# Kernel tuning notes

Measured on AMD Instinct MI355X. Metric: run time of the kernel, lower is better.

The kernel has to match this reference:

```python
import jax, jax.numpy as jnp
import numpy as np
from jax.ops import segment_sum, segment_max

B = 512          # parcels (batch of graphs)
P = 200          # poi nodes per parcel
N = B * P        # total poi nodes
E_POI = N * 16   # intra-parcel poi graph edges
HID = 256
IN_CH = 64
HEADS = 3
OUT = 12
T0 = 0.9
SLOPE = 0.2      # GATConv leaky_relu negative slope
NODE_GRAPH = jnp.arange(N, dtype=jnp.int32) // P  # poi node -> parcel id
ARANGE_N = jnp.arange(N, dtype=jnp.int32)


def setup_inputs() -> dict:
    key = jax.random.key(0)
    ks = jax.random.split(key, 24)
    g = lambda i, shape: jax.random.normal(ks[i], shape, jnp.float32) * 0.05
    # poi graph edges constrained within each parcel block
    src0 = jax.random.randint(ks[0], (E_POI,), 0, N, dtype=jnp.int32)
    off = jax.random.randint(ks[1], (E_POI,), 0, P, dtype=jnp.int32)
    return dict(
        g_poi_features=jax.random.normal(ks[2], (N, IN_CH), jnp.float32),
        img_feat=jax.random.normal(ks[3], (B, 2048), jnp.float32),
        edge_src=src0,
        edge_dst=(src0 // P) * P + off,
        W_gcn1=g(4, (IN_CH, HID)), b_gcn1=jnp.zeros((HID,), jnp.float32),
        W_gcn2=g(5, (HID, HID)), b_gcn2=jnp.zeros((HID,), jnp.float32),
        W_hrs=g(6, (2048, HID)), b_hrs=jnp.zeros((HID,), jnp.float32),
        W_proj_hrs=g(7, (HID, HID)), b_proj_hrs=jnp.zeros((HID,), jnp.float32),
        W_proj_poi=g(8, (HID, HID)), b_proj_poi=jnp.zeros((HID,), jnp.float32),
        W_gat_in=g(9, (HID, HEADS * HID)), al_in=g(10, (HEADS, HID)), ar_in=g(11, (HEADS, HID)),
        W_gat_with=g(12, (HID, HEADS * HID)), al_with=g(13, (HEADS, HID)), ar_with=g(14, (HEADS, HID)),
        W_hrsgnn=g(15, (HID, HID)),
        W_poignn=g(16, (HID, HID)),
        W_fc=g(17, (4 * HID, OUT)), b_fc=jnp.zeros((OUT,), jnp.float32),
    )


def _gcn(x, src, dst, W, b):
    # DGL GraphConv, norm='both', self-loops added
    s = jnp.concatenate([src, ARANGE_N])
    d = jnp.concatenate([dst, ARANGE_N])
    deg = segment_sum(jnp.ones_like(s, jnp.float32), d, num_segments=N)
    norm = jax.lax.rsqrt(jnp.maximum(deg, 1.0))
    h = (x @ W) * norm[:, None]
    m = segment_sum(h[s], d, num_segments=N)
    return m * norm[:, None] + b


def _gat(h_src, h_dst, src, dst, n_dst, W, al, ar):
    # DGL GATConv math: shared fc, additive attention, edge-softmax over dst
    fs = (h_src @ W).reshape(-1, HEADS, HID)
    fd = (h_dst @ W).reshape(-1, HEADS, HID)
    el = (fs * al).sum(-1)   # [n_src, H]
    er = (fd * ar).sum(-1)   # [n_dst, H]
    e = el[src] + er[dst]
    e = jnp.where(e > 0, e, SLOPE * e)
    m = segment_max(e, dst, num_segments=n_dst)
    w = jnp.exp(e - m[dst])
    z = segment_sum(w, dst, num_segments=n_dst)
    alpha = w / (z[dst] + 1e-9)
    out = segment_sum(fs[src] * alpha[:, :, None], dst, num_segments=n_dst)
    return out.mean(1)  # mean over heads (parcel_output.mean(1) in source)


def _mean_nodes(x):
    # dgl.mean_nodes over uniform-size batched graphs
    return segment_sum(x, NODE_GRAPH, num_segments=B) / P


def reference(g_poi_features, img_feat, edge_src, edge_dst,
              W_gcn1, b_gcn1, W_gcn2, b_gcn2, W_hrs, b_hrs,
              W_proj_hrs, b_proj_hrs, W_proj_poi, b_proj_poi,
              W_gat_in, al_in, ar_in, W_gat_with, al_with, ar_with,
              W_hrsgnn, W_poignn, W_fc, b_fc):
    # hrs_encoder: ResNet50 backbone modeled as precomputed 2048-d feats + replaced fc
    hrs = img_feat @ W_hrs + b_hrs                                  # [B, HID]
    # poi_encoder: 2-layer GCN over batched poi graph
    x = jax.nn.relu(_gcn(g_poi_features, edge_src, edge_dst, W_gcn1, b_gcn1))
    poi_nodes = _gcn(x, edge_src, edge_dst, W_gcn2, b_gcn2)         # [N, HID]
    poi_pooled = _mean_nodes(poi_nodes)                             # [B, HID]
    # mid-level fused similarity
    med = jnp.concatenate([hrs, poi_pooled], axis=1)
    med = med / jnp.linalg.norm(med, axis=1, keepdims=True)
    med_output = (med @ med.T + 1.0) / 2.0                          # [B, B]
    # UniSimGraph: GCN on thresholded parcel-similarity graph
    adj = jnp.where(med_output >= T0, 1.0, 0.0)
    adj = jnp.maximum(adj, jnp.eye(B, dtype=jnp.float32))
    dinv = jax.lax.rsqrt(adj.sum(1))
    nadj = adj * dinv[:, None] * dinv[None, :]
    hrs_agg = jax.nn.relu(nadj @ (hrs @ W_hrsgnn))                  # [B, HID]
    poi_agg = jax.nn.relu(nadj @ (poi_pooled @ W_poignn))           # [B, HID]
    # getHetGraph: bipartite poi<->parcel GAT, 3 heads, sum-aggregate, head-mean
    ph = hrs @ W_proj_hrs + b_proj_hrs                              # parcel feats
    pp = poi_nodes @ W_proj_poi + b_proj_poi                        # poi feats
    poi2img = _gat(pp, ph, ARANGE_N, NODE_GRAPH, B, W_gat_in, al_in, ar_in)      # [B, HID]
    img2poi = _gat(ph, pp, NODE_GRAPH, ARANGE_N, N, W_gat_with, al_with, ar_with)  # [N, HID]
    img2poi_pooled = _mean_nodes(img2poi)                           # [B, HID]
    # MutualAgg concat order: [img2poi, poi2poi(=poi_agg), poi2img, img2img(=hrs_agg)]
    agg = jnp.concatenate([img2poi_pooled, poi_agg, poi2img, hrs_agg], axis=1)
    output = agg @ W_fc + b_fc                                      # [B, OUT]
    return (output, med_output)
```

## Files before the change

kernel.cpp:

```cpp
#include <hip/hip_runtime.h>
#include <hip/hip_bf16.h>
#include <math.h>


#define N_NODES 102400
#define B_PAR   512
#define P_NODES 200
#define E_EDGES 1638400
#define HIDF    256

typedef __attribute__((ext_vector_type(8))) short bf16x8;
typedef __attribute__((ext_vector_type(4))) float f32x4;

__device__ __forceinline__ unsigned short f2bf(float x) {
    unsigned u = __builtin_bit_cast(unsigned, x);
    u += 0x7fffu + ((u >> 16) & 1u);
    return (unsigned short)(u >> 16);
}
__device__ __forceinline__ float bf2f(unsigned short h) {
    return __builtin_bit_cast(float, (unsigned)h << 16);
}
__device__ __forceinline__ int lds_off(int row, int kbyte) {
    return row * 128 + ((((kbyte >> 4) ^ (row & 7)) << 4) | (kbyte & 15));
}
template<bool BF16SRC>
__device__ __forceinline__ bf16x8 load_row8(const void* p, size_t elemoff) {
    if constexpr (BF16SRC) {
        return *(const bf16x8*)((const unsigned short*)p + elemoff);
    } else {
        const float* ap = (const float*)p + elemoff;
        float4 lo = *(const float4*)ap;
        float4 hi = *(const float4*)(ap + 4);
        union { bf16x8 v; unsigned short u[8]; } pk;
        pk.u[0] = f2bf(lo.x); pk.u[1] = f2bf(lo.y);
        pk.u[2] = f2bf(lo.z); pk.u[3] = f2bf(lo.w);
        pk.u[4] = f2bf(hi.x); pk.u[5] = f2bf(hi.y);
        pk.u[6] = f2bf(hi.z); pk.u[7] = f2bf(hi.w);
        return pk.v;
    }
}
__device__ __forceinline__ bf16x8 u8x8_to_bf16(uint2 w) {
    union { bf16x8 v; unsigned short u[8]; } r;
#pragma unroll
    for (int b = 0; b < 4; ++b) {
        r.u[b]     = (unsigned short)(__builtin_bit_cast(unsigned,
                        (float)((w.x >> (8 * b)) & 255u)) >> 16);
        r.u[4 + b] = (unsigned short)(__builtin_bit_cast(unsigned,
                        (float)((w.y >> (8 * b)) & 255u)) >> 16);
    }
    return r.v;
}

template<bool ABF16, bool BBF16, int OMODE, int SCMODE, bool BIASF, bool RELUF>
__global__ __launch_bounds__(512, 2) void mm256_k(
    const void* __restrict__ Ain, const void* __restrict__ Bin,
    void* __restrict__ Cout, int M, int Nc, int K,
    const float* __restrict__ scale, const float* __restrict__ bias)
{
    __shared__ bf16x8 smem_v[4096];
    unsigned char* Asm = (unsigned char*)smem_v;
    unsigned char* Bsm = Asm + 32768;

    const int tid  = threadIdx.x;
    const int m0   = blockIdx.y * 256;
    const int n0   = blockIdx.x * 256;
    const int sr   = tid >> 3, sc = tid & 7;
    const int lane = tid & 63;
    const int wave = tid >> 6;
    const int wm   = wave >> 2, wn = wave & 3;
    const int frow = lane & 15;
    const int fko  = (lane >> 4) << 4;

    f32x4 acc[8][4];
    const f32x4 fz = {0.f, 0.f, 0.f, 0.f};
#pragma unroll
    for (int i = 0; i < 8; ++i)
#pragma unroll
        for (int j = 0; j < 4; ++j) acc[i][j] = fz;

    bf16x8 areg[4], breg[4];
    auto load_tiles = [&](int k0) {
#pragma unroll
        for (int i = 0; i < 4; ++i) {
            int row = sr + 64 * i;
            areg[i] = load_row8<ABF16>(Ain, (size_t)(m0 + row) * K + k0 + sc * 8);
            breg[i] = load_row8<BBF16>(Bin, (size_t)(n0 + row) * K + k0 + sc * 8);
        }
    };

    load_tiles(0);
    for (int k0 = 0; k0 < K; k0 += 64) {
        __syncthreads();
#pragma unroll
        for (int i = 0; i < 4; ++i) {
            *(bf16x8*)(Asm + lds_off(sr + 64 * i, sc * 16)) = areg[i];
            *(bf16x8*)(Bsm + lds_off(sr + 64 * i, sc * 16)) = breg[i];
        }
        __syncthreads();
        if (k0 + 64 < K) load_tiles(k0 + 64);
#pragma unroll
        for (int ks = 0; ks < 2; ++ks) {
            const int kb = ks * 64 + fko;
            bf16x8 bfr[4];
#pragma unroll
            for (int t = 0; t < 4; ++t)
                bfr[t] = *(const bf16x8*)(Bsm + lds_off(wn * 64 + t * 16 + frow, kb));
#pragma unroll
            for (int mi = 0; mi < 8; ++mi) {
                bf16x8 af = *(const bf16x8*)(Asm + lds_off(wm * 128 + mi * 16 + frow, kb));
#pragma unroll
                for (int ni = 0; ni < 4; ++ni)
                    acc[mi][ni] = __builtin_amdgcn_mfma_f32_16x16x32_bf16(
                        af, bfr[ni], acc[mi][ni], 0, 0, 0);
            }
        }
    }

    const int r4 = (lane >> 4) << 2;
#pragma unroll
    for (int mi = 0; mi < 8; ++mi) {
#pragma unroll
        for (int ni = 0; ni < 4; ++ni) {
            int col = n0 + wn * 64 + ni * 16 + frow;
#pragma unroll
            for (int j = 0; j < 4; ++j) {
                int row = m0 + wm * 128 + mi * 16 + r4 + j;
                float v = acc[mi][ni][j];
                if (SCMODE == 1) v *= scale[row];
                if (SCMODE == 2) v *= scale[col];
                if (BIASF)       v += bias[col];
                if (RELUF)       v = fmaxf(v, 0.f);
                if (OMODE == 0) {
                    ((float*)Cout)[(size_t)row * Nc + col] = v;
                } else if (OMODE == 1) {
                    ((unsigned short*)Cout)[(size_t)row * Nc + col] = f2bf(v);
                } else {
                    int p = col / 200, r = col - p * 200;
                    ((unsigned short*)Cout)[((size_t)p * 256 + row) * 256 + r] = f2bf(v);
                }
            }
        }
    }
}

__global__ __launch_bounds__(512, 2) void agg256_k(
    const unsigned char* __restrict__ Adj, const unsigned short* __restrict__ Yt,
    unsigned short* __restrict__ Outb, const float* __restrict__ nrm,
    const float* __restrict__ bias, int relu)
{
    __shared__ bf16x8 smem_v[4096];
    unsigned char* Asm = (unsigned char*)smem_v;
    unsigned char* Bsm = Asm + 32768;

    const int tid  = threadIdx.x;
    const int p    = blockIdx.x;
    const int sr   = tid >> 3, sc = tid & 7;
    const int lane = tid & 63;
    const int wave = tid >> 6;
    const int wm   = wave >> 2, wn = wave & 3;
    const int frow = lane & 15;
    const int fko  = (lane >> 4) << 4;
    const size_t abase = (size_t)p * 65536;
    const size_t ybase = (size_t)p * 65536;

    f32x4 acc[8][4];
    const f32x4 fz = {0.f, 0.f, 0.f, 0.f};
#pragma unroll
    for (int i = 0; i < 8; ++i)
#pragma unroll
        for (int j = 0; j < 4; ++j) acc[i][j] = fz;

    uint2  awreg[4];
    bf16x8 breg[4];
    auto load_tiles = [&](int k0) {
#pragma unroll
        for (int i = 0; i < 4; ++i) {
            int row = sr + 64 * i;
            awreg[i] = *(const uint2*)(Adj + abase + (size_t)row * 256 + k0 + sc * 8);
            breg[i]  = *(const bf16x8*)(Yt + ybase + (size_t)row * 256 + k0 + sc * 8);
        }
    };

    load_tiles(0);
#pragma unroll
    for (int t4 = 0; t4 < 4; ++t4) {
        __syncthreads();
#pragma unroll
        for (int i = 0; i < 4; ++i) {
            *(bf16x8*)(Asm + lds_off(sr + 64 * i, sc * 16)) = u8x8_to_bf16(awreg[i]);
            *(bf16x8*)(Bsm + lds_off(sr + 64 * i, sc * 16)) = breg[i];
        }
        __syncthreads();
        if (t4 < 3) load_tiles((t4 + 1) * 64);
#pragma unroll
        for (int ks = 0; ks < 2; ++ks) {
            const int kb = ks * 64 + fko;
            bf16x8 bfr[4];
#pragma unroll
            for (int t = 0; t < 4; ++t)
                bfr[t] = *(const bf16x8*)(Bsm + lds_off(wn * 64 + t * 16 + frow, kb));
#pragma unroll
            for (int mi = 0; mi < 8; ++mi) {
                bf16x8 af = *(const bf16x8*)(Asm + lds_off(wm * 128 + mi * 16 + frow, kb));
#pragma unroll
                for (int ni = 0; ni < 4; ++ni)
                    acc[mi][ni] = __builtin_amdgcn_mfma_f32_16x16x32_bf16(
                        af, bfr[ni], acc[mi][ni], 0, 0, 0);
            }
        }
    }

    const int r4 = (lane >> 4) << 2;
#pragma unroll
    for (int mi = 0; mi < 8; ++mi) {
#pragma unroll
        for (int ni = 0; ni < 4; ++ni) {
            int col = wn * 64 + ni * 16 + frow;
#pragma unroll
            for (int j = 0; j < 4; ++j) {
                int d = wm * 128 + mi * 16 + r4 + j;
                if (d < 200) {
                    int g = p * 200 + d;
                    float v = acc[mi][ni][j] * nrm[g] + bias[col];
                    if (relu) v = fmaxf(v, 0.f);
                    Outb[(size_t)g * 256 + col] = f2bf(v);
                }
            }
        }
    }
}

__global__ __launch_bounds__(512) void agg1_k(
    const unsigned char* __restrict__ Adj, const unsigned short* __restrict__ Xnt,
    unsigned short* __restrict__ AX)
{
    __shared__ bf16x8 smem_v[2560];
    unsigned char* Asm = (unsigned char*)smem_v;
    unsigned char* Bsm = Asm + 32768;

    const int tid  = threadIdx.x;
    const int p    = blockIdx.x;
    const int arow = tid >> 1, ah = tid & 1;
    const int brow = tid >> 3, sc = tid & 7;
    const int lane = tid & 63;
    const int wave = tid >> 6;
    const int frow = lane & 15;
    const int fko  = (lane >> 4) << 4;
    const size_t abase = (size_t)p * 65536;
    const size_t xbase = (size_t)p * 16384;

    f32x4 acc[2][4];
    const f32x4 fz = {0.f, 0.f, 0.f, 0.f};
#pragma unroll
    for (int i = 0; i < 2; ++i)
#pragma unroll
        for (int j = 0; j < 4; ++j) acc[i][j] = fz;

    uint4  aw[2];
    bf16x8 bg;
    auto load_tiles = [&](int k0) {
        const uint4* ap = (const uint4*)(Adj + abase + (size_t)arow * 256 + k0 + ah * 32);
        aw[0] = ap[0];
        aw[1] = ap[1];
        bg = *(const bf16x8*)(Xnt + xbase + (size_t)brow * 256 + k0 + sc * 8);
    };

    load_tiles(0);
#pragma unroll
    for (int t4 = 0; t4 < 4; ++t4) {
        __syncthreads();
        {
            uint2 l0 = {aw[0].x, aw[0].y}, h0 = {aw[0].z, aw[0].w};
            uint2 l1 = {aw[1].x, aw[1].y}, h1 = {aw[1].z, aw[1].w};
            int base = ah * 64;
            *(bf16x8*)(Asm + lds_off(arow, base +  0)) = u8x8_to_bf16(l0);
            *(bf16x8*)(Asm + lds_off(arow, base + 16)) = u8x8_to_bf16(h0);
            *(bf16x8*)(Asm + lds_off(arow, base + 32)) = u8x8_to_bf16(l1);
            *(bf16x8*)(Asm + lds_off(arow, base + 48)) = u8x8_to_bf16(h1);
            *(bf16x8*)(Bsm + lds_off(brow, sc * 16)) = bg;
        }
        __syncthreads();
        if (t4 < 3) load_tiles((t4 + 1) * 64);
#pragma unroll
        for (int ks = 0; ks < 2; ++ks) {
            const int kb = ks * 64 + fko;
            bf16x8 bfr[4];
#pragma unroll
            for (int t = 0; t < 4; ++t)
                bfr[t] = *(const bf16x8*)(Bsm + lds_off(t * 16 + frow, kb));
#pragma unroll
            for (int mi = 0; mi < 2; ++mi) {
                bf16x8 af = *(const bf16x8*)(Asm + lds_off(wave * 32 + mi * 16 + frow, kb));
#pragma unroll
                for (int ni = 0; ni < 4; ++ni)
                    acc[mi][ni] = __builtin_amdgcn_mfma_f32_16x16x32_bf16(
                        af, bfr[ni], acc[mi][ni], 0, 0, 0);
            }
        }
    }

    const int r4 = (lane >> 4) << 2;
#pragma unroll
    for (int mi = 0; mi < 2; ++mi) {
#pragma unroll
        for (int ni = 0; ni < 4; ++ni) {
            int col = ni * 16 + frow;
#pragma unroll
            for (int j = 0; j < 4; ++j) {
                int d = wave * 32 + mi * 16 + r4 + j;
                if (d < 200)
                    AX[((size_t)(p * 200 + d)) * 64 + col] = f2bf(acc[mi][ni][j]);
            }
        }
    }
}

__global__ __launch_bounds__(256) void xt_k(const float* __restrict__ gp,
                                            const float* __restrict__ nrm,
                                            unsigned short* __restrict__ Xnt)
{
    __shared__ unsigned short lsh[64][264];
    const int p = blockIdx.x, tid = threadIdx.x;
    for (int idx = tid; idx < 256 * 16; idx += 256) {
        int s = idx >> 4, kc = idx & 15;
        float4 v = {0.f, 0.f, 0.f, 0.f};
        float nr = 0.f;
        if (s < 200) {
            v = *(const float4*)(gp + ((size_t)(p * 200 + s)) * 64 + kc * 4);
            nr = nrm[p * 200 + s];
        }
        lsh[kc * 4 + 0][s] = f2bf(v.x * nr);
        lsh[kc * 4 + 1][s] = f2bf(v.y * nr);
        lsh[kc * 4 + 2][s] = f2bf(v.z * nr);
        lsh[kc * 4 + 3][s] = f2bf(v.w * nr);
    }
    __syncthreads();
    for (int idx = tid; idx < 64 * 32; idx += 256) {
        int k = idx >> 5, ch = idx & 31;
        uint4 o = *(const uint4*)(&lsh[k][ch * 8]);
        *(uint4*)(Xnt + (size_t)p * 16384 + k * 256 + ch * 8) = o;
    }
}

template<bool ABF16, bool BBF16, int OMODE, bool BIASF, bool RELUF,
         bool MEDOUT, int KCHUNK>
__global__ __launch_bounds__(256) void mm64_k(
    const void* __restrict__ Ain, const void* __restrict__ Bin,
    void* __restrict__ Cout, int M, int Nc, int K,
    const float* __restrict__ bias, float alpha)
{
    __shared__ bf16x8 smem_v[1024];
    unsigned char* Asm = (unsigned char*)smem_v;
    unsigned char* Bsm = Asm + 8192;

    const int tid  = threadIdx.x;
    const int m0   = blockIdx.y * 64;
    const int n0   = blockIdx.x * 64;
    const int sr   = tid >> 3, sc = tid & 7;
    const int lane = tid & 63;
    const int wm   = (tid >> 7) & 1, wn = (tid >> 6) & 1;
    const int frow = lane & 15;
    const int fko  = (lane >> 4) << 4;

    int kbeg = 0, kend = K;
    float* Cf = (float*)Cout;
    if (KCHUNK > 0) {
        kbeg = blockIdx.z * KCHUNK; kend = kbeg + KCHUNK;
        Cf += (size_t)blockIdx.z * M * Nc;
    }

    f32x4 acc[2][2];
    const f32x4 fz = {0.f, 0.f, 0.f, 0.f};
#pragma unroll
    for (int i = 0; i < 2; ++i)
#pragma unroll
        for (int j = 0; j < 2; ++j) acc[i][j] = fz;

    bf16x8 areg[2], breg[2];
    auto load_tiles = [&](int k0) {
#pragma unroll
        for (int i = 0; i < 2; ++i) {
            int row = sr + 32 * i;
            areg[i] = load_row8<ABF16>(Ain, (size_t)(m0 + row) * K + k0 + sc * 8);
            breg[i] = load_row8<BBF16>(Bin, (size_t)(n0 + row) * K + k0 + sc * 8);
        }
    };

    load_tiles(kbeg);
    for (int k0 = kbeg; k0 < kend; k0 += 64) {
        __syncthreads();
#pragma unroll
        for (int i = 0; i < 2; ++i) {
            *(bf16x8*)(Asm + lds_off(sr + 32 * i, sc * 16)) = areg[i];
            *(bf16x8*)(Bsm + lds_off(sr + 32 * i, sc * 16)) = breg[i];
        }
        __syncthreads();
        if (k0 + 64 < kend) load_tiles(k0 + 64);
#pragma unroll
        for (int ks = 0; ks < 2; ++ks) {
            const int kb = ks * 64 + fko;
            bf16x8 af[2], bfr[2];
#pragma unroll
            for (int t = 0; t < 2; ++t)
                af[t] = *(const bf16x8*)(Asm + lds_off(wm * 32 + t * 16 + frow, kb));
#pragma unroll
            for (int t = 0; t < 2; ++t)
                bfr[t] = *(const bf16x8*)(Bsm + lds_off(wn * 32 + t * 16 + frow, kb));
#pragma unroll
            for (int mi = 0; mi < 2; ++mi)
#pragma unroll
                for (int ni = 0; ni < 2; ++ni)
                    acc[mi][ni] = __builtin_amdgcn_mfma_f32_16x16x32_bf16(
                        af[mi], bfr[ni], acc[mi][ni], 0, 0, 0);
        }
    }

    const int r4 = (lane >> 4) << 2;
#pragma unroll
    for (int mi = 0; mi < 2; ++mi) {
#pragma unroll
        for (int ni = 0; ni < 2; ++ni) {
            int col = n0 + wn * 32 + ni * 16 + frow;
#pragma unroll
// ... 54 lines not shown
__global__ __launch_bounds__(256) void prep_k(
    const float* __restrict__ W1, const float* __restrict__ W2,
    const float* __restrict__ Whg,
    const float* __restrict__ Wpg, const float* __restrict__ Whrs,
    const float* __restrict__ Wgin, const float* __restrict__ Wgw,
    const float* __restrict__ Wph, const float* __restrict__ img,
    unsigned short* __restrict__ W1t, unsigned short* __restrict__ W2t,
    unsigned short* __restrict__ Whgt,
    unsigned short* __restrict__ Wpgt, unsigned short* __restrict__ Whrst,
    unsigned short* __restrict__ Wgint, unsigned short* __restrict__ Wmt,
    unsigned short* __restrict__ Wphb, unsigned short* __restrict__ imgb)
{
    int b = blockIdx.x, tid = threadIdx.x;
    if (b < 64) {
        int id = b * 256 + tid; int n = id >> 6, k = id & 63;
        W1t[id] = f2bf(W1[(size_t)k * 256 + n]);
    } else if (b < 320) {
        int id = (b - 64) * 256 + tid; int n = id >> 8, k = id & 255;
        W2t[id] = f2bf(W2[(size_t)k * 256 + n]);
    } else if (b < 576) {
        int id = (b - 320) * 256 + tid; int n = id >> 8, k = id & 255;
        Whgt[id] = f2bf(Whg[(size_t)k * 256 + n]);
    } else if (b < 832) {
        int id = (b - 576) * 256 + tid; int n = id >> 8, k = id & 255;
        Wpgt[id] = f2bf(Wpg[(size_t)k * 256 + n]);
    } else if (b < 2880) {
        int id = (b - 832) * 256 + tid; int n = id >> 11, k = id & 2047;
        Whrst[id] = f2bf(Whrs[(size_t)k * 256 + n]);
    } else if (b < 3648) {
        int id = (b - 2880) * 256 + tid; int j = id / 768, k2 = id - j * 768;
        int t = k2 & 255, h = k2 >> 8;
        Wgint[id] = f2bf(Wgin[(size_t)t * 768 + h * 256 + j]);
    } else if (b < 3904) {
        int id = (b - 3648) * 256 + tid; int j = id >> 8, t = id & 255;
        const float c3 = (1.f / 3.f) * (1.f / (1.f + 1e-9f));
        float s = Wgw[(size_t)t * 768 + j] + Wgw[(size_t)t * 768 + 256 + j] +
                  Wgw[(size_t)t * 768 + 512 + j];
        Wmt[id] = f2bf(s * c3);
    } else if (b < 4160) {
        int id = (b - 3904) * 256 + tid;
        Wphb[id] = f2bf(Wph[id]);
    } else {
        int id = (b - 4160) * 256 + tid;
        imgb[id] = f2bf(img[id]);
    }
}

__global__ __launch_bounds__(256) void wpg_k(
    const float* __restrict__ Wpp, const float* __restrict__ Wgin,
    const float* __restrict__ bpp,
    unsigned short* __restrict__ WpG, float* __restrict__ bgg)
{
    __shared__ float wsh[256];
    const int b = blockIdx.x, j = threadIdx.x;
    if (b < 768) {
        int h = b >> 8, c = b & 255;
        wsh[j] = Wpp[(size_t)c * 256 + j];
        __syncthreads();
        float acc = 0.f;
        for (int t = 0; t < 256; ++t)
            acc += wsh[t] * Wgin[(size_t)t * 768 + h * 256 + j];
        WpG[(size_t)j * 768 + h * 256 + c] = f2bf(acc);
    } else {
        float s = 0.f;
        for (int h = 0; h < 3; ++h)
            for (int t = 0; t < 256; ++t)
                s += bpp[t] * Wgin[(size_t)t * 768 + h * 256 + j];
        bgg[j] = s * (1.f / 3.f);
    }
}

__global__ __launch_bounds__(256) void hrs_reduce_k(
    const float* __restrict__ part, const float* __restrict__ bhrs,
    float* __restrict__ hrs, unsigned short* __restrict__ hrsb)
{
    int id = blockIdx.x * 256 + threadIdx.x;
    float s = bhrs[id & 255];
#pragma unroll
    for (int z = 0; z < 8; ++z) s += part[(size_t)z * 131072 + id];
    hrs[id] = s;
    hrsb[id] = f2bf(s);
}

__global__ __launch_bounds__(256) void pool_k(const unsigned short* __restrict__ X,
                                              float* __restrict__ Pl,
                                              unsigned short* __restrict__ Plb)
{
    __shared__ float sh[2048];
    const int b = blockIdx.x, tid = threadIdx.x;
    const int cg = tid & 31, rg = tid >> 5;
    const size_t base = (size_t)b * P_NODES * HIDF + cg * 8;
    float acc[8] = {};
    for (int n = rg; n < P_NODES; n += 8) {
        union { uint4 q; unsigned short u[8]; } v;
        v.q = *(const uint4*)(X + base + (size_t)n * HIDF);
#pragma unroll
        for (int j = 0; j < 8; ++j) acc[j] += bf2f(v.u[j]);
    }
#pragma unroll
    for (int j = 0; j < 8; ++j) sh[rg * 256 + cg * 8 + j] = acc[j];
    __syncthreads();
    float s = 0.f;
#pragma unroll
    for (int r = 0; r < 8; ++r) s += sh[r * 256 + tid];
    s *= (1.f / 200.f);
    Pl[(size_t)b * 256 + tid] = s;
    Plb[(size_t)b * 256 + tid] = f2bf(s);
}

__global__ __launch_bounds__(256) void med_build_k(
    const float* __restrict__ hrs, const float* __restrict__ pool,
    unsigned short* __restrict__ medb)
{
    __shared__ float red[256];
    int b = blockIdx.x, f = threadIdx.x;
    float v0 = hrs[(size_t)b * 256 + f];
    float v1 = pool[(size_t)b * 256 + f];
    red[f] = v0 * v0 + v1 * v1;
    __syncthreads();
    for (int s = 128; s > 0; s >>= 1) {
        if (f < s) red[f] += red[f + s];
        __syncthreads();
    }
    float inv = rsqrtf(red[0]);
    medb[(size_t)b * 512 + f]       = f2bf(v0 * inv);
    medb[(size_t)b * 512 + 256 + f] = f2bf(v1 * inv);
}

__global__ __launch_bounds__(256) void dinv_k(const float* __restrict__ mo,
                                              float* __restrict__ dinv)
{
    __shared__ int red[256];
    int i = blockIdx.x, t = threadIdx.x;
    int c = 0;
    for (int j = t; j < 512; j += 256) c += (mo[(size_t)i * 512 + j] >= 0.9f) ? 1 : 0;
    red[t] = c; __syncthreads();
    for (int s = 128; s > 0; s >>= 1) {
        if (t < s) red[t] += red[t + s];
        __syncthreads();
    }
    if (t == 0) dinv[i] = rsqrtf((float)red[0]);
}

__global__ __launch_bounds__(256) void nadj_k(const float* __restrict__ mo,
                                              const float* __restrict__ dinv,
                                              unsigned short* __restrict__ nadjb)
{
    int i = blockIdx.x, t = threadIdx.x;
    float di = dinv[i];
    for (int j = t; j < 512; j += 256) {
        float a = (mo[(size_t)i * 512 + j] >= 0.9f || j == i) ? 1.f : 0.f;
        nadjb[(size_t)i * 512 + j] = f2bf(a * di * dinv[j]);
    }
}

__global__ __launch_bounds__(256) void uv1_k(
    const float* __restrict__ Wgin, const float* __restrict__ al,
    const float* __restrict__ ar,
    float* __restrict__ u2, float* __restrict__ v2)
{
    const int wave = threadIdx.x >> 6, lane = threadIdx.x & 63;
    const int task = blockIdx.x * 4 + wave;
    const int k = task / 3, h = task - k * 3;
    float4 w = *(const float4*)(Wgin + (size_t)k * 768 + h * 256 + lane * 4);
    float4 a = *(const float4*)(al + h * 256 + lane * 4);
    float4 r = *(const float4*)(ar + h * 256 + lane * 4);
    float su = w.x * a.x + w.y * a.y + w.z * a.z + w.w * a.w;
    float sv = w.x * r.x + w.y * r.y + w.z * r.z + w.w * r.w;
#pragma unroll
    for (int o = 32; o > 0; o >>= 1) {
        su += __shfl_xor(su, o);
        sv += __shfl_xor(sv, o);
    }
    if (lane == 0) { u2[task] = su; v2[task] = sv; }
}

__global__ __launch_bounds__(256) void uv2_k(
    const float* __restrict__ Wph, const float* __restrict__ Wpp,
    const float* __restrict__ bph, const float* __restrict__ bpp,
    const unsigned short* __restrict__ Wmt,
    const float* __restrict__ u2, const float* __restrict__ v2,
    float* __restrict__ vv2, float* __restrict__ wu,
    float* __restrict__ bc, float* __restrict__ erb, float* __restrict__ eb0)
{
    __shared__ float ush[768], vsh[768];
    const int tid = threadIdx.x;
    for (int i = tid; i < 768; i += 256) { ush[i] = u2[i]; vsh[i] = v2[i]; }
    __syncthreads();
    const int wave = tid >> 6, lane = tid & 63;
    const int task = blockIdx.x * 4 + wave;
    float s = 0.f;
    if (task < 1536) {
// ... 88 lines not shown
        float sm = 0.f;
        for (int n = lane; n < P_NODES; n += 64) sm += expf(esh[n * 3 + wave] - mx);
        for (int o = 32; o > 0; o >>= 1) sm += __shfl_xor(sm, o);
        if (lane == 0) { mz[wave] = mx; mz[4 + wave] = sm; }
    }
    __syncthreads();

    for (int it = tid; it < 600; it += 256) {
        int h = it % 3;
        ash[it] = expf(esh[it] - mz[h]) / (mz[4 + h] + 1e-9f);
    }
    __syncthreads();

    float a0 = 0.f, a1 = 0.f, a2 = 0.f;
    for (int n = 0; n < P_NODES; ++n) {
        float vv = bf2f(PN[(base + n) * HIDF + tid]);
        a0 += ash[n * 3 + 0] * vv;
        a1 += ash[n * 3 + 1] * vv;
        a2 += ash[n * 3 + 2] * vv;
    }
    q[((size_t)p * 3 + 0) * 256 + tid] = a0;
    q[((size_t)p * 3 + 1) * 256 + tid] = a1;
    q[((size_t)p * 3 + 2) * 256 + tid] = a2;
}

__global__ __launch_bounds__(256) void final_k(
    const float* __restrict__ i2p, const float* __restrict__ hpagg,
    const float* __restrict__ p2i,
    const float* __restrict__ Wfc, const float* __restrict__ bfc,
    float* __restrict__ out)
{
    int id = blockIdx.x * 256 + threadIdx.x;
    if (id >= B_PAR * 12) return;
    int b = id / 12, o = id % 12;
    float acc = bfc[o];
    const float* s0 = i2p + (size_t)b * 256;
    const float* s1 = hpagg + (size_t)b * 512 + 256;
    const float* s2 = p2i + (size_t)b * 256;
    const float* s3 = hpagg + (size_t)b * 512;
    for (int k = 0; k < 256; ++k) {
        acc += s0[k] * Wfc[(size_t)(0 * 256 + k) * 12 + o];
        acc += s1[k] * Wfc[(size_t)(1 * 256 + k) * 12 + o];
        acc += s2[k] * Wfc[(size_t)(2 * 256 + k) * 12 + o];
        acc += s3[k] * Wfc[(size_t)(3 * 256 + k) * 12 + o];
    }
    out[id] = acc;
}

extern "C" void kernel_launch(void* const* d_in, const int* in_sizes, int n_in,
                              void* d_out, int out_size, void* d_ws, size_t ws_size,
                              hipStream_t stream)
{
    const float* g_poi = (const float*)d_in[0];
    const float* img   = (const float*)d_in[1];
    const int*   esrc  = (const int*)d_in[2];
    const int*   edst  = (const int*)d_in[3];
    const float* W1    = (const float*)d_in[4];
    const float* b1    = (const float*)d_in[5];
    const float* W2    = (const float*)d_in[6];
    const float* b2    = (const float*)d_in[7];
    const float* Whrs  = (const float*)d_in[8];
    const float* bhrs  = (const float*)d_in[9];
    const float* Wph   = (const float*)d_in[10];
    const float* bph   = (const float*)d_in[11];
    const float* Wpp   = (const float*)d_in[12];
    const float* bpp   = (const float*)d_in[13];
    const float* Wgin  = (const float*)d_in[14];
    const float* alin  = (const float*)d_in[15];
    const float* arin  = (const float*)d_in[16];
    const float* Wgw   = (const float*)d_in[17];
    const float* Whg   = (const float*)d_in[20];
    const float* Wpg   = (const float*)d_in[21];
    const float* Wfc   = (const float*)d_in[22];
    const float* bfc   = (const float*)d_in[23];

    float* out     = (float*)d_out;
    float* med_out = out + B_PAR * 12;

    char* ws = (char*)d_ws;
    size_t off = 0;
    auto take = [&](size_t bytes) { void* pv = ws + off; off += (bytes + 255) & ~(size_t)255; return pv; };

    unsigned char*  adj8 = (unsigned char*)take((size_t)B_PAR * 256 * 256);
    unsigned short* Yt   = (unsigned short*)take((size_t)B_PAR * 256 * 256 * 2);
    unsigned short* Xnt  = Yt;
    unsigned short* XPN  = (unsigned short*)take((size_t)N_NODES * 256 * 2);
    unsigned short* AX   = (unsigned short*)take((size_t)N_NODES * 64 * 2);
    float*          part = (float*)take((size_t)8 * 512 * 256 * 4);

    unsigned short* W1t   = (unsigned short*)take(256 * 64 * 2);
    unsigned short* W2t   = (unsigned short*)take(256 * 256 * 2);
    unsigned short* Whgt  = (unsigned short*)take(256 * 256 * 2);
    unsigned short* Wpgt  = (unsigned short*)take(256 * 256 * 2);
    unsigned short* Whrst = (unsigned short*)take((size_t)256 * 2048 * 2);
    unsigned short* Wgint = (unsigned short*)take((size_t)256 * 768 * 2);
    unsigned short* Wmt   = (unsigned short*)take(256 * 256 * 2);
    unsigned short* Wphb  = (unsigned short*)take(256 * 256 * 2);
    unsigned short* WcT   = (unsigned short*)take(256 * 256 * 2);
    unsigned short* WpG   = (unsigned short*)take((size_t)256 * 768 * 2);
    unsigned short* imgb  = (unsigned short*)take((size_t)512 * 2048 * 2);
    unsigned short* hrsb  = (unsigned short*)take((size_t)B_PAR * 256 * 2);
    unsigned short* poolb = (unsigned short*)take((size_t)B_PAR * 256 * 2);
    unsigned short* medb  = (unsigned short*)take((size_t)B_PAR * 512 * 2);
    unsigned short* nadjb = (unsigned short*)take((size_t)B_PAR * 512 * 2);
    unsigned short* Tcatt = (unsigned short*)take((size_t)512 * 512 * 2);
    float* nrm   = (float*)take((size_t)N_NODES * 4);
    float* hrs   = (float*)take((size_t)B_PAR * 256 * 4);
    float* pool  = (float*)take((size_t)B_PAR * 256 * 4);
    float* dinv  = (float*)take((size_t)B_PAR * 4);
    float* hpagg = (float*)take((size_t)B_PAR * 512 * 4);
    float* u2    = (float*)take(768 * 4);
    float* v2    = (float*)take(768 * 4);
    float* wu    = (float*)take(768 * 4);
    float* vv2   = (float*)take(768 * 4);
    float* erb   = (float*)take(16);
    float* eb0   = (float*)take(16);
    float* bc    = (float*)take(256 * 4);
    float* bgg   = (float*)take(256 * 4);
    float* er    = (float*)take((size_t)B_PAR * 3 * 4);
    float* q     = (float*)take((size_t)B_PAR * 768 * 4);
    float* p2i   = (float*)take((size_t)B_PAR * 256 * 4);
    float* i2p   = (float*)take((size_t)B_PAR * 256 * 4);
    (void)ws_size; (void)in_sizes; (void)n_in; (void)out_size;

    hipMemsetAsync(adj8, 0, (size_t)B_PAR * 256 * 256, stream);
    prep_k<<<8256, 256, 0, stream>>>(W1, W2, Whg, Wpg, Whrs, Wgin, Wgw,
        Wph, img, W1t, W2t, Whgt, Wpgt, Whrst, Wgint, Wmt, Wphb, imgb);
    edge_diag_k<<<(E_EDGES + N_NODES) / 256, 256, 0, stream>>>(esrc, edst, adj8);
    norm2_k<<<N_NODES / 256, 256, 0, stream>>>(adj8, nrm);
    wpg_k<<<769, 256, 0, stream>>>(Wpp, Wgin, bpp, WpG, bgg);

    mm64_k<true, true, 0, false, false, false, 256>
        <<<dim3(4, 8, 8), 256, 0, stream>>>(imgb, Whrst, part, 512, 256, 2048,
            nullptr, 1.f);
    hrs_reduce_k<<<512, 256, 0, stream>>>(part, bhrs, hrs, hrsb);

    uv1_k<<<192, 256, 0, stream>>>(Wgin, alin, arin, u2, v2);
    uv2_k<<<450, 256, 0, stream>>>(Wph, Wpp, bph, bpp, Wmt, u2, v2,
                                   vv2, wu, bc, erb, eb0);
    er2_k<<<384, 256, 0, stream>>>(hrs, vv2, erb, eb0, er);
    mm64_k<true, true, 1, false, false, false, 0>
        <<<dim3(4, 4), 256, 0, stream>>>(Wmt, Wphb, WcT, 256, 256, 256,
            nullptr, 1.f);

    xt_k<<<512, 256, 0, stream>>>(g_poi, nrm, Xnt);
    agg1_k<<<512, 512, 0, stream>>>(adj8, Xnt, AX);
    mm256_k<true, true, 1, 1, true, true>
        <<<dim3(1, 400), 512, 0, stream>>>(AX, W1t, XPN, N_NODES, 256, 64,
            nrm, b1);

    mm256_k<true, true, 2, 2, false, false>
        <<<dim3(400, 1), 512, 0, stream>>>(W2t, XPN, Yt, 256, N_NODES, 256,
            nrm, nullptr);
    agg256_k<<<512, 512, 0, stream>>>(adj8, Yt, XPN, nrm, b2, 0);

    pool_k<<<B_PAR, 256, 0, stream>>>(XPN, pool, poolb);

    med_build_k<<<B_PAR, 256, 0, stream>>>(hrs, pool, medb);
    mm64_k<true, true, 0, false, false, true, 0>
        <<<dim3(8, 8), 256, 0, stream>>>(medb, medb, med_out, 512, 512, 512,
            nullptr, 0.5f);

    dinv_k<<<B_PAR, 256, 0, stream>>>(med_out, dinv);
    nadj_k<<<B_PAR, 256, 0, stream>>>(med_out, dinv, nadjb);
    mm64_k<true, true, 1, false, false, false, 0>
        <<<dim3(8, 4), 256, 0, stream>>>(Whgt, hrsb, Tcatt, 256, 512, 256,
            nullptr, 1.f);
    mm64_k<true, true, 1, false, false, false, 0>
        <<<dim3(8, 4), 256, 0, stream>>>(Wpgt, poolb, Tcatt + (size_t)256 * 512,
            256, 512, 256, nullptr, 1.f);
    mm64_k<true, true, 0, false, true, false, 0>
        <<<dim3(8, 8), 256, 0, stream>>>(nadjb, Tcatt, hpagg, 512, 512, 512,
            nullptr, 1.f);

    gat_poi2img_k<<<B_PAR, 256, 0, stream>>>(XPN, wu, er, q);
    mm64_k<false, true, 0, true, false, false, 0>
        <<<dim3(4, 8), 256, 0, stream>>>(q, WpG, p2i, 512, 256, 768,
            bgg, 1.f / 3.f);

    mm64_k<true, true, 0, true, false, false, 0>
        <<<dim3(4, 8), 256, 0, stream>>>(hrsb, WcT, i2p, 512, 256, 256,
            bc, 1.f);

    final_k<<<24, 256, 0, stream>>>(i2p, hpagg, p2i, Wfc, bfc, out);
}
```

Measured before the change: 428.2 us.

## Fuse GCN layers into per-parcel kernels with in-LDS aggregation and pooling

Replaces the xt/agg1/mm256/agg256/pool kernel chain with two per-parcel kernels. gcnA does transpose-normalize, adjacency aggregation and the W1 projection with bias/relu in one block and writes a normalized transposed layer-1 output. gcnB aggregates over the adjacency first and then multiplies by W2 in K-chunks, with mean pooling fused into its epilogue. This removes intermediate global buffers and several launches, and cuts the K extent to 224 instead of 256. In exchange each block carries heavy register and LDS use and fine-grained syncs, which may lower occupancy.

Result: faster. 391.6 us (-8.5%).

```diff
diff --git a/kernel.cpp b/kernel.cpp
--- a/kernel.cpp
+++ b/kernel.cpp
@@ -51,277 +51,42 @@
     return r.v;
 }
 
-template<bool ABF16, bool BBF16, int OMODE, int SCMODE, bool BIASF, bool RELUF>
-__global__ __launch_bounds__(512, 2) void mm256_k(
-    const void* __restrict__ Ain, const void* __restrict__ Bin,
-    void* __restrict__ Cout, int M, int Nc, int K,
-    const float* __restrict__ scale, const float* __restrict__ bias)
-{
-    __shared__ bf16x8 smem_v[4096];
-    unsigned char* Asm = (unsigned char*)smem_v;
-    unsigned char* Bsm = Asm + 32768;
-
-    const int tid  = threadIdx.x;
-    const int m0   = blockIdx.y * 256;
-    const int n0   = blockIdx.x * 256;
-    const int sr   = tid >> 3, sc = tid & 7;
-    const int lane = tid & 63;
-    const int wave = tid >> 6;
-    const int wm   = wave >> 2, wn = wave & 3;
-    const int frow = lane & 15;
-    const int fko  = (lane >> 4) << 4;
-
-    f32x4 acc[8][4];
-    const f32x4 fz = {0.f, 0.f, 0.f, 0.f};
-#pragma unroll
-    for (int i = 0; i < 8; ++i)
-#pragma unroll
-        for (int j = 0; j < 4; ++j) acc[i][j] = fz;
-
-    bf16x8 areg[4], breg[4];
-    auto load_tiles = [&](int k0) {
-#pragma unroll
-        for (int i = 0; i < 4; ++i) {
-            int row = sr + 64 * i;
-            areg[i] = load_row8<ABF16>(Ain, (size_t)(m0 + row) * K + k0 + sc * 8);
-            breg[i] = load_row8<BBF16>(Bin, (size_t)(n0 + row) * K + k0 + sc * 8);
-        }
-    };
-
-    load_tiles(0);
-    for (int k0 = 0; k0 < K; k0 += 64) {
-        __syncthreads();
-#pragma unroll
-        for (int i = 0; i < 4; ++i) {
-            *(bf16x8*)(Asm + lds_off(sr + 64 * i, sc * 16)) = areg[i];
-            *(bf16x8*)(Bsm + lds_off(sr + 64 * i, sc * 16)) = breg[i];
-        }
-        __syncthreads();
-        if (k0 + 64 < K) load_tiles(k0 + 64);
-#pragma unroll
-        for (int ks = 0; ks < 2; ++ks) {
-            const int kb = ks * 64 + fko;
-            bf16x8 bfr[4];
-#pragma unroll
-            for (int t = 0; t < 4; ++t)
-                bfr[t] = *(const bf16x8*)(Bsm + lds_off(wn * 64 + t * 16 + frow, kb));
-#pragma unroll
-            for (int mi = 0; mi < 8; ++mi) {
-                bf16x8 af = *(const bf16x8*)(Asm + lds_off(wm * 128 + mi * 16 + frow, kb));
-#pragma unroll
-                for (int ni = 0; ni < 4; ++ni)
-                    acc[mi][ni] = __builtin_amdgcn_mfma_f32_16x16x32_bf16(
-                        af, bfr[ni], acc[mi][ni], 0, 0, 0);
-            }
-        }
-    }
-
-    const int r4 = (lane >> 4) << 2;
-#pragma unroll
-    for (int mi = 0; mi < 8; ++mi) {
-#pragma unroll
-        for (int ni = 0; ni < 4; ++ni) {
-            int col = n0 + wn * 64 + ni * 16 + frow;
-#pragma unroll
-            for (int j = 0; j < 4; ++j) {
-                int row = m0 + wm * 128 + mi * 16 + r4 + j;
-                float v = acc[mi][ni][j];
-                if (SCMODE == 1) v *= scale[row];
-                if (SCMODE == 2) v *= scale[col];
-                if (BIASF)       v += bias[col];
-                if (RELUF)       v = fmaxf(v, 0.f);
-                if (OMODE == 0) {
-                    ((float*)Cout)[(size_t)row * Nc + col] = v;
-                } else if (OMODE == 1) {
-                    ((unsigned short*)Cout)[(size_t)row * Nc + col] = f2bf(v);
-                } else {
-                    int p = col / 200, r = col - p * 200;
-                    ((unsigned short*)Cout)[((size_t)p * 256 + row) * 256 + r] = f2bf(v);
-                }
-            }
-        }
-    }
-}
-
-__global__ __launch_bounds__(512, 2) void agg256_k(
-    const unsigned char* __restrict__ Adj, const unsigned short* __restrict__ Yt,
-    unsigned short* __restrict__ Outb, const float* __restrict__ nrm,
-    const float* __restrict__ bias, int relu)
-{
-    __shared__ bf16x8 smem_v[4096];
-    unsigned char* Asm = (unsigned char*)smem_v;
-    unsigned char* Bsm = Asm + 32768;
+__global__ __launch_bounds__(512, 2) void gcnA_k(
+    const unsigned char* __restrict__ Adj, const float* __restrict__ gp,
+    const float* __restrict__ nrm, const unsigned short* __restrict__ W1t,
+    const float* __restrict__ b1, unsigned short* __restrict__ X1nT)
+{
+    __shared__ unsigned short lds[256 * 72];
+    unsigned short* XnT = lds;
+    unsigned short* AX1 = lds;
 
     const int tid  = threadIdx.x;
     const int p    = blockIdx.x;
-    const int sr   = tid >> 3, sc = tid & 7;
-    const int lane = tid & 63;
-    const int wave = tid >> 6;
-    const int wm   = wave >> 2, wn = wave & 3;
-    const int frow = lane & 15;
-    const int fko  = (lane >> 4) << 4;
-    const size_t abase = (size_t)p * 65536;
-    const size_t ybase = (size_t)p * 65536;
-
-    f32x4 acc[8][4];
-    const f32x4 fz = {0.f, 0.f, 0.f, 0.f};
-#pragma unroll
-    for (int i = 0; i < 8; ++i)
-#pragma unroll
-        for (int j = 0; j < 4; ++j) acc[i][j] = fz;
-
-    uint2  awreg[4];
-    bf16x8 breg[4];
-    auto load_tiles = [&](int k0) {
-#pragma unroll
-        for (int i = 0; i < 4; ++i) {
-            int row = sr + 64 * i;
-            awreg[i] = *(const uint2*)(Adj + abase + (size_t)row * 256 + k0 + sc * 8);
-            breg[i]  = *(const bf16x8*)(Yt + ybase + (size_t)row * 256 + k0 + sc * 8);
-        }
-    };
-
-    load_tiles(0);
-#pragma unroll
-    for (int t4 = 0; t4 < 4; ++t4) {
-        __syncthreads();
-#pragma unroll
-        for (int i = 0; i < 4; ++i) {
-            *(bf16x8*)(Asm + lds_off(sr + 64 * i, sc * 16)) = u8x8_to_bf16(awreg[i]);
-            *(bf16x8*)(Bsm + lds_off(sr + 64 * i, sc * 16)) = breg[i];
-        }
-        __syncthreads();
-        if (t4 < 3) load_tiles((t4 + 1) * 64);
-#pragma unroll
-        for (int ks = 0; ks < 2; ++ks) {
-            const int kb = ks * 64 + fko;
-            bf16x8 bfr[4];
-#pragma unroll
-            for (int t = 0; t < 4; ++t)
-                bfr[t] = *(const bf16x8*)(Bsm + lds_off(wn * 64 + t * 16 + frow, kb));
-#pragma unroll
-            for (int mi = 0; mi < 8; ++mi) {
-                bf16x8 af = *(const bf16x8*)(Asm + lds_off(wm * 128 + mi * 16 + frow, kb));
-#pragma unroll
-                for (int ni = 0; ni < 4; ++ni)
-                    acc[mi][ni] = __builtin_amdgcn_mfma_f32_16x16x32_bf16(
-                        af, bfr[ni], acc[mi][ni], 0, 0, 0);
-            }
-        }
-    }
-
-    const int r4 = (lane >> 4) << 2;
-#pragma unroll
-    for (int mi = 0; mi < 8; ++mi) {
-#pragma unroll
-        for (int ni = 0; ni < 4; ++ni) {
-            int col = wn * 64 + ni * 16 + frow;
-#pragma unroll
-            for (int j = 0; j < 4; ++j) {
-                int d = wm * 128 + mi * 16 + r4 + j;
-                if (d < 200) {
-                    int g = p * 200 + d;
-                    float v = acc[mi][ni][j] * nrm[g] + bias[col];
-                    if (relu) v = fmaxf(v, 0.f);
-                    Outb[(size_t)g * 256 + col] = f2bf(v);
-                }
-            }
-        }
-    }
-}
-
-__global__ __launch_bounds__(512) void agg1_k(
-    const unsigned char* __restrict__ Adj, const unsigned short* __restrict__ Xnt,
-    unsigned short* __restrict__ AX)
-{
-    __shared__ bf16x8 smem_v[2560];
-    unsigned char* Asm = (unsigned char*)smem_v;
-    unsigned char* Bsm = Asm + 32768;
-
-    const int tid  = threadIdx.x;
-    const int p    = blockIdx.x;
-    const int arow = tid >> 1, ah = tid & 1;
-    const int brow = tid >> 3, sc = tid & 7;
     const int lane = tid & 63;
     const int wave = tid >> 6;
     const int frow = lane & 15;
-    const int fko  = (lane >> 4) << 4;
-    const size_t abase = (size_t)p * 65536;
-    const size_t xbase = (size_t)p * 16384;
-
-    f32x4 acc[2][4];
+    const int fq   = lane >> 4;
+    const int r4   = fq << 2;
     const f32x4 fz = {0.f, 0.f, 0.f, 0.f};
-#pragma unroll
-    for (int i = 0; i < 2; ++i)
-#pragma unroll
-        for (int j = 0; j < 4; ++j) acc[i][j] = fz;
-
-    uint4  aw[2];
-    bf16x8 bg;
-    auto load_tiles = [&](int k0) {
-        const uint4* ap = (const uint4*)(Adj + abase + (size_t)arow * 256 + k0 + ah * 32);
-        aw[0] = ap[0];
-        aw[1] = ap[1];
-        bg = *(const bf16x8*)(Xnt + xbase + (size_t)brow * 256 + k0 + sc * 8);
-    };
-
-    load_tiles(0);
-#pragma unroll
-    for (int t4 = 0; t4 < 4; ++t4) {
-        __syncthreads();
-        {
-            uint2 l0 = {aw[0].x, aw[0].y}, h0 = {aw[0].z, aw[0].w};
-            uint2 l1 = {aw[1].x, aw[1].y}, h1 = {aw[1].z, aw[1].w};
-            int base = ah * 64;
-            *(bf16x8*)(Asm + lds_off(arow, base +  0)) = u8x8_to_bf16(l0);
-            *(bf16x8*)(Asm + lds_off(arow, base + 16)) = u8x8_to_bf16(h0);
-            *(bf16x8*)(Asm + lds_off(arow, base + 32)) = u8x8_to_bf16(l1);
-            *(bf16x8*)(Asm + lds_off(arow, base + 48)) = u8x8_to_bf16(h1);
-            *(bf16x8*)(Bsm + lds_off(brow, sc * 16)) = bg;
-        }
-        __syncthreads();
-        if (t4 < 3) load_tiles((t4 + 1) * 64);
-#pragma unroll
-        for (int ks = 0; ks < 2; ++ks) {
-            const int kb = ks * 64 + fko;
-            bf16x8 bfr[4];
-#pragma unroll
-            for (int t = 0; t < 4; ++t)
-                bfr[t] = *(const bf16x8*)(Bsm + lds_off(t * 16 + frow, kb));
-#pragma unroll
-            for (int mi = 0; mi < 2; ++mi) {
-                bf16x8 af = *(const bf16x8*)(Asm + lds_off(wave * 32 + mi * 16 + frow, kb));
-#pragma unroll
-                for (int ni = 0; ni < 4; ++ni)
-                    acc[mi][ni] = __builtin_amdgcn_mfma_f32_16x16x32_bf16(
-                        af, bfr[ni], acc[mi][ni], 0, 0, 0);
-            }
-        }
-    }
-
-    const int r4 = (lane >> 4) << 2;
+
+    uint2 adjr[2][7];
 #pragma unroll
     for (int mi = 0; mi < 2; ++mi) {
-#pragma unroll
-        for (int ni = 0; ni < 4; ++ni) {
-            int col = ni * 16 + frow;
-#pragma unroll
-            for (int j = 0; j < 4; ++j) {
-                int d = wave * 32 + mi * 16 + r4 + j;
-                if (d < 200)
-                    AX[((size_t)(p * 200 + d)) * 64 + col] = f2bf(acc[mi][ni][j]);
-            }
-        }
-    }
-}
-
-__global__ __launch_bounds__(256) void xt_k(const float* __restrict__ gp,
-                                            const float* __restrict__ nrm,
-                                            unsigned short* __restrict__ Xnt)
-{
-    __shared__ unsigned short lsh[64][264];
-    const int p = blockIdx.x, tid = threadIdx.x;
-    for (int idx = tid; idx < 256 * 16; idx += 256) {
+        const unsigned char* ar = Adj + ((size_t)p << 16)
+            + (size_t)(wave * 32 + mi * 16 + frow) * 256 + fq * 8;
+#pragma unroll
+        for (int ks = 0; ks < 7; ++ks)
+            adjr[mi][ks] = *(const uint2*)(ar + ks * 32);
+    }
+    bf16x8 w1f[2][2];
+#pragma unroll
+    for (int mi = 0; mi < 2; ++mi)
+#pragma unroll
+        for (int ks = 0; ks < 2; ++ks)
+            w1f[mi][ks] = *(const bf16x8*)(W1t
+                + (size_t)(wave * 32 + mi * 16 + frow) * 64 + ks * 32 + fq * 8);
+
+    for (int idx = tid; idx < 224 * 16; idx += 512) {
         int s = idx >> 4, kc = idx & 15;
         float4 v = {0.f, 0.f, 0.f, 0.f};
         float nr = 0.f;
@@ -329,16 +94,235 @@
             v = *(const float4*)(gp + ((size_t)(p * 200 + s)) * 64 + kc * 4);
             nr = nrm[p * 200 + s];
         }
-        lsh[kc * 4 + 0][s] = f2bf(v.x * nr);
-        lsh[kc * 4 + 1][s] = f2bf(v.y * nr);
-        lsh[kc * 4 + 2][s] = f2bf(v.z * nr);
-        lsh[kc * 4 + 3][s] = f2bf(v.w * nr);
-    }
-    __syncthreads();
-    for (int idx = tid; idx < 64 * 32; idx += 256) {
-        int k = idx >> 5, ch = idx & 31;
-        uint4 o = *(const uint4*)(&lsh[k][ch * 8]);
-        *(uint4*)(Xnt + (size_t)p * 16384 + k * 256 + ch * 8) = o;
+        XnT[(kc * 4 + 0) * 232 + s] = f2bf(v.x * nr);
+        XnT[(kc * 4 + 1) * 232 + s] = f2bf(v.y * nr);
+        XnT[(kc * 4 + 2) * 232 + s] = f2bf(v.z * nr);
+        XnT[(kc * 4 + 3) * 232 + s] = f2bf(v.w * nr);
+    }
+    __syncthreads();
+
+    f32x4 acc2[2][4];
+#pragma unroll
+    for (int i = 0; i < 2; ++i)
+#pragma unroll
+        for (int j = 0; j < 4; ++j) acc2[i][j] = fz;
+#pragma unroll
+    for (int ks = 0; ks < 7; ++ks) {
+        bf16x8 a0 = u8x8_to_bf16(adjr[0][ks]);
+        bf16x8 a1 = u8x8_to_bf16(adjr[1][ks]);
+#pragma unroll
+        for (int ni = 0; ni < 4; ++ni) {
+            bf16x8 bfr = *(const bf16x8*)(XnT
+                + (size_t)(ni * 16 + frow) * 232 + ks * 32 + fq * 8);
+            acc2[0][ni] = __builtin_amdgcn_mfma_f32_16x16x32_bf16(a0, bfr, acc2[0][ni], 0, 0, 0);
+            acc2[1][ni] = __builtin_amdgcn_mfma_f32_16x16x32_bf16(a1, bfr, acc2[1][ni], 0, 0, 0);
+        }
+    }
+    __syncthreads();
+#pragma unroll
+    for (int mi = 0; mi < 2; ++mi)
+#pragma unroll
+        for (int ni = 0; ni < 4; ++ni)
+#pragma unroll
+            for (int j = 0; j < 4; ++j)
+                AX1[(size_t)(wave * 32 + mi * 16 + r4 + j) * 72 + ni * 16 + frow]
+                    = f2bf(acc2[mi][ni][j]);
+    __syncthreads();
+
+    f32x4 acc3[2][16];
+#pragma unroll
+    for (int i = 0; i < 2; ++i)
+#pragma unroll
+        for (int j = 0; j < 16; ++j) acc3[i][j] = fz;
+#pragma unroll
+    for (int ks = 0; ks < 2; ++ks)
+#pragma unroll
+        for (int ni = 0; ni < 16; ++ni) {
+            bf16x8 bfr = *(const bf16x8*)(AX1
+                + (size_t)(ni * 16 + frow) * 72 + ks * 32 + fq * 8);
+            acc3[0][ni] = __builtin_amdgcn_mfma_f32_16x16x32_bf16(w1f[0][ks], bfr, acc3[0][ni], 0, 0, 0);
+            acc3[1][ni] = __builtin_amdgcn_mfma_f32_16x16x32_bf16(w1f[1][ks], bfr, acc3[1][ni], 0, 0, 0);
+        }
+
+    float nrd[16];
+#pragma unroll
+    for (int ni = 0; ni < 16; ++ni) {
+        int d = ni * 16 + frow;
+        nrd[ni] = (d < 200) ? nrm[p * 200 + d] : 0.f;
+    }
+#pragma unroll
+    for (int mi = 0; mi < 2; ++mi)
+#pragma unroll
+        for (int j = 0; j < 4; ++j) {
+            int f = wave * 32 + mi * 16 + r4 + j;
+            float bv = b1[f];
+#pragma unroll
+            for (int ni = 0; ni < 16; ++ni) {
+                int d = ni * 16 + frow;
+                if (d < 224) {
+                    float v = fmaxf(acc3[mi][ni][j] * nrd[ni] + bv, 0.f) * nrd[ni];
+                    X1nT[((size_t)p * 256 + f) * 224 + d] = f2bf(v);
+                }
+            }
+        }
+}
+
+__global__ __launch_bounds__(512, 2) void gcnB_k(
+    const unsigned char* __restrict__ Adj, const unsigned short* __restrict__ X1nT,
+    const unsigned short* __restrict__ W2t, const float* __restrict__ nrm,
+    const float* __restrict__ b2, unsigned short* __restrict__ PN,
+    float* __restrict__ pool, unsigned short* __restrict__ poolb)
+{
+    __shared__ unsigned short Bb[32 * 232];
+    __shared__ unsigned short AXb[256 * 40];
+    __shared__ unsigned short W2b[256 * 40];
+    __shared__ float poolsh[256];
+
+    const int tid  = threadIdx.x;
+    const int p    = blockIdx.x;
+    const int lane = tid & 63;
+    const int wave = tid >> 6;
+    const int frow = lane & 15;
+    const int fq   = lane >> 4;
+    const int r4   = fq << 2;
+    const f32x4 fz = {0.f, 0.f, 0.f, 0.f};
+
+    if (tid < 256) poolsh[tid] = 0.f;
+
+    bf16x8 adjb[2][7];
+#pragma unroll
+    for (int mi = 0; mi < 2; ++mi) {
+        const unsigned char* ar = Adj + ((size_t)p << 16)
+            + (size_t)(wave * 32 + mi * 16 + frow) * 256 + fq * 8;
+#pragma unroll
+        for (int ks = 0; ks < 7; ++ks)
+            adjb[mi][ks] = u8x8_to_bf16(*(const uint2*)(ar + ks * 32));
+    }
+
+    f32x4 acc5[2][16];
+#pragma unroll
+    for (int i = 0; i < 2; ++i)
+#pragma unroll
+        for (int j = 0; j < 16; ++j) acc5[i][j] = fz;
+
+#pragma unroll
+    for (int i = 0; i < 2; ++i) {
+        int idx = tid + i * 512;
+        if (idx < 896) {
+            int r = idx / 28, ch = idx - r * 28;
+            *(uint4*)(Bb + r * 232 + ch * 8) =
+                *(const uint4*)(X1nT + ((size_t)p * 256 + r) * 224 + ch * 8);
+        }
+        int r2 = idx >> 2, ch2 = idx & 3;
+        *(uint4*)(W2b + r2 * 40 + ch2 * 8) =
+            *(const uint4*)(W2t + (size_t)r2 * 256 + ch2 * 8);
+    }
+    __syncthreads();
+
+    for (int c = 0; c < 8; ++c) {
+        uint4 stb[2];
+#pragma unroll
+        for (int i = 0; i < 2; ++i) {
+            int idx = tid + i * 512;
+            if (c < 7 && idx < 896) {
+                int r = idx / 28, ch = idx - r * 28;
+                stb[i] = *(const uint4*)(X1nT
+                    + ((size_t)p * 256 + (c + 1) * 32 + r) * 224 + ch * 8);
+            }
+        }
+        f32x4 acc4[2][2];
+#pragma unroll
+        for (int i = 0; i < 2; ++i)
+#pragma unroll
+            for (int j = 0; j < 2; ++j) acc4[i][j] = fz;
+#pragma unroll
+        for (int ks = 0; ks < 7; ++ks)
+#pragma unroll
+            for (int ni = 0; ni < 2; ++ni) {
+                bf16x8 bfr = *(const bf16x8*)(Bb
+                    + (size_t)(ni * 16 + frow) * 232 + ks * 32 + fq * 8);
+                acc4[0][ni] = __builtin_amdgcn_mfma_f32_16x16x32_bf16(adjb[0][ks], bfr, acc4[0][ni], 0, 0, 0);
+                acc4[1][ni] = __builtin_amdgcn_mfma_f32_16x16x32_bf16(adjb[1][ks], bfr, acc4[1][ni], 0, 0, 0);
+            }
+        __syncthreads();
+#pragma unroll
+        for (int mi = 0; mi < 2; ++mi)
+#pragma unroll
+            for (int ni = 0; ni < 2; ++ni)
+#pragma unroll
+                for (int j = 0; j < 4; ++j)
+                    AXb[(size_t)(wave * 32 + mi * 16 + r4 + j) * 40 + ni * 16 + frow]
+                        = f2bf(acc4[mi][ni][j]);
+#pragma unroll
+        for (int i = 0; i < 2; ++i) {
+            int idx = tid + i * 512;
+            if (c < 7 && idx < 896) {
+                int r = idx / 28, ch = idx - r * 28;
+                *(uint4*)(Bb + r * 232 + ch * 8) = stb[i];
+            }
+        }
+        __syncthreads();
+        uint4 stw[2];
+#pragma unroll
+        for (int i = 0; i < 2; ++i) {
+            int idx = tid + i * 512;
+            int r = idx >> 2, ch = idx & 3;
+            if (c < 7)
+                stw[i] = *(const uint4*)(W2t
+                    + (size_t)r * 256 + (c + 1) * 32 + ch * 8);
+        }
+        bf16x8 af[2];
+        af[0] = *(const bf16x8*)(AXb + (size_t)(wave * 32 + frow) * 40 + fq * 8);
+        af[1] = *(const bf16x8*)(AXb + (size_t)(wave * 32 + 16 + frow) * 40 + fq * 8);
+#pragma unroll
+        for (int ni = 0; ni < 16; ++ni) {
+            bf16x8 bfr = *(const bf16x8*)(W2b + (size_t)(ni * 16 + frow) * 40 + fq * 8);
+            acc5[0][ni] = __builtin_amdgcn_mfma_f32_16x16x32_bf16(af[0], bfr, acc5[0][ni], 0, 0, 0);
+            acc5[1][ni] = __builtin_amdgcn_mfma_f32_16x16x32_bf16(af[1], bfr, acc5[1][ni], 0, 0, 0);
+        }
+        __syncthreads();
+#pragma unroll
+        for (int i = 0; i < 2; ++i) {
+            int idx = tid + i * 512;
+            int r = idx >> 2, ch = idx & 3;
+            if (c < 7) *(uint4*)(W2b + r * 40 + ch * 8) = stw[i];
+        }
+    }
+
+    float b2v[16], psum[16];
+#pragma unroll
+    for (int ni = 0; ni < 16; ++ni) {
+        b2v[ni] = b2[ni * 16 + frow];
+        psum[ni] = 0.f;
+    }
+#pragma unroll
+    for (int mi = 0; mi < 2; ++mi)
+#pragma unroll
+        for (int j = 0; j < 4; ++j) {
+            int d = wave * 32 + mi * 16 + r4 + j;
+            if (d < 200) {
+                int g = p * 200 + d;
+                float nr = nrm[g];
+#pragma unroll
+                for (int ni = 0; ni < 16; ++ni) {
+                    float v = acc5[mi][ni][j] * nr + b2v[ni];
+                    PN[(size_t)g * 256 + ni * 16 + frow] = f2bf(v);
+                    psum[ni] += v;
+                }
+            }
+        }
+#pragma unroll
+    for (int ni = 0; ni < 16; ++ni) {
+        float s = psum[ni];
+        s += __shfl_xor(s, 16);
+        s += __shfl_xor(s, 32);
+        if (fq == 0) atomicAdd(&poolsh[ni * 16 + frow], s);
+    }
+    __syncthreads();
+    if (tid < 256) {
+        float pv = poolsh[tid] * (1.f / 200.f);
+        pool[(size_t)p * 256 + tid] = pv;
+        poolb[(size_t)p * 256 + tid] = f2bf(pv);
     }
 }
 
@@ -559,32 +543,6 @@
     hrsb[id] = f2bf(s);
 }
 
-__global__ __launch_bounds__(256) void pool_k(const unsigned short* __restrict__ X,
-                                              float* __restrict__ Pl,
-                                              unsigned short* __restrict__ Plb)
-{
-    __shared__ float sh[2048];
-    const int b = blockIdx.x, tid = threadIdx.x;
-    const int cg = tid & 31, rg = tid >> 5;
-    const size_t base = (size_t)b * P_NODES * HIDF + cg * 8;
-    float acc[8] = {};
-    for (int n = rg; n < P_NODES; n += 8) {
-        union { uint4 q; unsigned short u[8]; } v;
-        v.q = *(const uint4*)(X + base + (size_t)n * HIDF);
-#pragma unroll
-        for (int j = 0; j < 8; ++j) acc[j] += bf2f(v.u[j]);
-    }
-#pragma unroll
-    for (int j = 0; j < 8; ++j) sh[rg * 256 + cg * 8 + j] = acc[j];
-    __syncthreads();
-    float s = 0.f;
-#pragma unroll
-    for (int r = 0; r < 8; ++r) s += sh[r * 256 + tid];
-    s *= (1.f / 200.f);
-    Pl[(size_t)b * 256 + tid] = s;
-    Plb[(size_t)b * 256 + tid] = f2bf(s);
-}
-
 __global__ __launch_bounds__(256) void med_build_k(
     const float* __restrict__ hrs, const float* __restrict__ pool,
     unsigned short* __restrict__ medb)
@@ -839,10 +797,8 @@
     auto take = [&](size_t bytes) { void* pv = ws + off; off += (bytes + 255) & ~(size_t)255; return pv; };
 
     unsigned char*  adj8 = (unsigned char*)take((size_t)B_PAR * 256 * 256);
-    unsigned short* Yt   = (unsigned short*)take((size_t)B_PAR * 256 * 256 * 2);
-    unsigned short* Xnt  = Yt;
+    unsigned short* X1nT = (unsigned short*)take((size_t)B_PAR * 256 * 224 * 2);
     unsigned short* XPN  = (unsigned short*)take((size_t)N_NODES * 256 * 2);
-    unsigned short* AX   = (unsigned short*)take((size_t)N_NODES * 64 * 2);
     float*          part = (float*)take((size_t)8 * 512 * 256 * 4);
 
     unsigned short* W1t   = (unsigned short*)take(256 * 64 * 2);
@@ -900,18 +856,9 @@
         <<<dim3(4, 4), 256, 0, stream>>>(Wmt, Wphb, WcT, 256, 256, 256,
             nullptr, 1.f);
 
-    xt_k<<<512, 256, 0, stream>>>(g_poi, nrm, Xnt);
-    agg1_k<<<512, 512, 0, stream>>>(adj8, Xnt, AX);
-    mm256_k<true, true, 1, 1, true, true>
-        <<<dim3(1, 400), 512, 0, stream>>>(AX, W1t, XPN, N_NODES, 256, 64,
-            nrm, b1);
-
-    mm256_k<true, true, 2, 2, false, false>
-        <<<dim3(400, 1), 512, 0, stream>>>(W2t, XPN, Yt, 256, N_NODES, 256,
-            nrm, nullptr);
-    agg256_k<<<512, 512, 0, stream>>>(adj8, Yt, XPN, nrm, b2, 0);
-
-    pool_k<<<B_PAR, 256, 0, stream>>>(XPN, pool, poolb);
+    gcnA_k<<<B_PAR, 512, 0, stream>>>(adj8, g_poi, nrm, W1t, b1, X1nT);
+    gcnB_k<<<B_PAR, 512, 0, stream>>>(adj8, X1nT, W2t, nrm, b2, XPN,
+                                      pool, poolb);
 
     med_build_k<<<B_PAR, 256, 0, stream>>>(hrs, pool, medb);
     mm64_k<true, true, 0, false, false, true, 0>
```
